# Kernel tuning notes

Measured on AMD Instinct MI355X. Metric: run time of the kernel, lower is better.

## Reference

```python
import jax, jax.numpy as jnp
import numpy as np

D_MODEL = 1024
N_HEADS = 16
D_K = D_MODEL // N_HEADS
BATCH = 8
SEQ = 1024
ROPE_BASE = 10000.0


def setup_inputs() -> dict:
    key = jax.random.key(0)
    ks = jax.random.split(key, 9)
    s = 1.0 / np.sqrt(D_MODEL)
    return {
        "x": jax.random.normal(ks[0], (BATCH, SEQ, D_MODEL), dtype=jnp.float32),
        "position_ids": jnp.arange(SEQ, dtype=jnp.int32)[None, :],
        "Wq": jax.random.normal(ks[1], (D_MODEL, D_MODEL), dtype=jnp.float32) * s,
        "bq": jnp.zeros((D_MODEL,), dtype=jnp.float32),
        "Wk": jax.random.normal(ks[2], (D_MODEL, D_MODEL), dtype=jnp.float32) * s,
        "bk": jnp.zeros((D_MODEL,), dtype=jnp.float32),
        "Wv": jax.random.normal(ks[3], (D_MODEL, D_MODEL), dtype=jnp.float32) * s,
        "bv": jnp.zeros((D_MODEL,), dtype=jnp.float32),
        "Wo": jax.random.normal(ks[4], (D_MODEL, D_MODEL), dtype=jnp.float32) * s,
        "bo": jnp.zeros((D_MODEL,), dtype=jnp.float32),
    }


def _apply_rope(t, position_ids):
    # t: [B, H, S, D_K]; position_ids: [1, S] (broadcast over batch)
    half = D_K // 2
    inv_freq = 1.0 / (ROPE_BASE ** (jnp.arange(half, dtype=jnp.float32) * 2.0 / D_K))
    ang = position_ids.astype(jnp.float32)[..., None] * inv_freq  # [1, S, half]
    cos = jnp.cos(ang)[:, None, :, :]  # [1, 1, S, half]
    sin = jnp.sin(ang)[:, None, :, :]
    t1, t2 = jnp.split(t, 2, axis=-1)
    return jnp.concatenate([t1 * cos - t2 * sin, t1 * sin + t2 * cos], axis=-1)


def reference(x, position_ids, Wq, bq, Wk, bk, Wv, bv, Wo, bo):
    B, S, D = x.shape
    def proj(W, b):
        # torch Linear: x @ W.T + b
        y = jnp.einsum('bsd,ed->bse', x, W) + b
        return y.reshape(B, S, N_HEADS, D_K).transpose(0, 2, 1, 3)  # [B,H,S,Dk]
    Q = proj(Wq, bq)
    K = proj(Wk, bk)
    V = proj(Wv, bv)
    Q = _apply_rope(Q, position_ids)
    K = _apply_rope(K, position_ids)
    scores = jnp.einsum('bhqd,bhkd->bhqk', Q, K) / jnp.sqrt(jnp.float32(D_K))
    attn = jax.nn.softmax(scores, axis=-1)
    out = jnp.einsum('bhqk,bhkd->bhqd', attn, V)
    out = out.transpose(0, 2, 1, 3).reshape(B, S, D)
    return jnp.einsum('bsd,ed->bse', out, Wo) + bo
```

## Files before the change

### kernel.cpp

```cpp
#include <hip/hip_runtime.h>
#include <hip/hip_bf16.h>


typedef __bf16 bf16_t;
typedef __bf16 bf16x8 __attribute__((ext_vector_type(8)));
typedef float  f32x4  __attribute__((ext_vector_type(4)));

static __device__ __forceinline__ f32x4 mfma16(bf16x8 a, bf16x8 b, f32x4 c) {
  return __builtin_amdgcn_mfma_f32_16x16x32_bf16(a, b, c, 0, 0, 0);
}

#if __has_builtin(__builtin_amdgcn_exp2f)
#define EXP2F(x) __builtin_amdgcn_exp2f(x)
#else
#define EXP2F(x) exp2f(x)
#endif

__global__ void k_prep(const float* __restrict__ x, const float* __restrict__ Wq,
                       const float* __restrict__ Wk, const float* __restrict__ Wv,
                       const float* __restrict__ Wo, const int* __restrict__ pos,
                       bf16_t* __restrict__ Xf, bf16_t* __restrict__ Wf,
                       float2* __restrict__ rt) {
  const int bid = blockIdx.x;
  const int t = threadIdx.x;
  if (bid < 4096) {
    int g = bid * 256 + t;
    int rg = g >> 11, kt = (g >> 6) & 31, lane = g & 63;
    int m = rg * 16 + (lane & 15);
    int k = kt * 32 + (lane >> 4) * 8;
    const float* s = x + (size_t)m * 1024 + k;
    float4 v0 = *(const float4*)s;
    float4 v1 = *(const float4*)(s + 4);
    union { bf16_t b[8]; } pk;
    pk.b[0] = (bf16_t)v0.x; pk.b[1] = (bf16_t)v0.y; pk.b[2] = (bf16_t)v0.z; pk.b[3] = (bf16_t)v0.w;
    pk.b[4] = (bf16_t)v1.x; pk.b[5] = (bf16_t)v1.y; pk.b[6] = (bf16_t)v1.z; pk.b[7] = (bf16_t)v1.w;
    __builtin_memcpy(Xf + (size_t)g * 8, pk.b, 16);
  } else if (bid < 6144) {
    int g = (bid - 4096) * 256 + t;
    int rg = g >> 11, kt = (g >> 6) & 31, lane = g & 63;
    const float* src = (rg < 64) ? Wq : (rg < 128) ? Wk : (rg < 192) ? Wv : Wo;
    int row = (rg & 63) * 16 + (lane & 15);
    int k = kt * 32 + (lane >> 4) * 8;
    const float* s = src + (size_t)row * 1024 + k;
    float4 v0 = *(const float4*)s;
    float4 v1 = *(const float4*)(s + 4);
    union { bf16_t b[8]; } pk;
    pk.b[0] = (bf16_t)v0.x; pk.b[1] = (bf16_t)v0.y; pk.b[2] = (bf16_t)v0.z; pk.b[3] = (bf16_t)v0.w;
    pk.b[4] = (bf16_t)v1.x; pk.b[5] = (bf16_t)v1.y; pk.b[6] = (bf16_t)v1.z; pk.b[7] = (bf16_t)v1.w;
    __builtin_memcpy(Wf + (size_t)g * 8, pk.b, 16);
  } else {
    int rb = bid - 6144;
    int s = rb * 8 + (t >> 5);
    int f = t & 31;
    float p = (float)pos[s];
    float inv = powf(10000.0f, -(float)(2 * f) / 64.0f);
    float a = p * inv;
    rt[s * 32 + f] = make_float2(cosf(a), sinf(a));
  }
}

#define GEMM_DIRECT_BODY(AfBase, BfBase)                                       \
  const int t = threadIdx.x;                                                   \
  const int lane = t & 63, w = t >> 6;                                         \
  const int hi = lane >> 4, c = lane & 15;                                     \
  const int wm = w >> 2, wn = w & 3;                                           \
  const bf16_t* Ab = (AfBase) + (size_t)((i0 >> 4) + wm * 4) * 16384 + lane * 8; \
  const bf16_t* Bb = (BfBase) + (size_t)((e0 >> 4) + wn * 4) * 16384 + lane * 8; \
  bf16x8 pa0, pa1, pa2, pa3, pb0, pb1, pb2, pb3;                               \
  bf16x8 qa0, qa1, qa2, qa3, qb0, qb1, qb2, qb3;                               \
  f32x4 acc[4][4] = {};                                                        \
  auto loadP = [&](int kt) {                                                   \
    pa0 = *(const bf16x8*)(Ab + kt * 512);                                     \
    pa1 = *(const bf16x8*)(Ab + 16384 + kt * 512);                             \
    pa2 = *(const bf16x8*)(Ab + 32768 + kt * 512);                             \
    pa3 = *(const bf16x8*)(Ab + 49152 + kt * 512);                             \
    pb0 = *(const bf16x8*)(Bb + kt * 512);                                     \
    pb1 = *(const bf16x8*)(Bb + 16384 + kt * 512);                             \
    pb2 = *(const bf16x8*)(Bb + 32768 + kt * 512);                             \
    pb3 = *(const bf16x8*)(Bb + 49152 + kt * 512);                             \
  };                                                                           \
  auto loadQ = [&](int kt) {                                                   \
    qa0 = *(const bf16x8*)(Ab + kt * 512);                                     \
    qa1 = *(const bf16x8*)(Ab + 16384 + kt * 512);                             \
    qa2 = *(const bf16x8*)(Ab + 32768 + kt * 512);                             \
    qa3 = *(const bf16x8*)(Ab + 49152 + kt * 512);                             \
    qb0 = *(const bf16x8*)(Bb + kt * 512);                                     \
    qb1 = *(const bf16x8*)(Bb + 16384 + kt * 512);                             \
    qb2 = *(const bf16x8*)(Bb + 32768 + kt * 512);                             \
    qb3 = *(const bf16x8*)(Bb + 49152 + kt * 512);                             \
  };                                                                           \
  auto compP = [&]() {                                                         \
    bf16x8 a_[4] = {pa0, pa1, pa2, pa3}, b_[4] = {pb0, pb1, pb2, pb3};         \
    __builtin_amdgcn_s_setprio(1);                                             \
    _Pragma("unroll") for (int fr = 0; fr < 4; ++fr)                           \
      _Pragma("unroll") for (int nc = 0; nc < 4; ++nc)                         \
        acc[fr][nc] = mfma16(a_[fr], b_[nc], acc[fr][nc]);                     \
    __builtin_amdgcn_s_setprio(0);                                             \
  };                                                                           \
  auto compQ = [&]() {                                                         \
    bf16x8 a_[4] = {qa0, qa1, qa2, qa3}, b_[4] = {qb0, qb1, qb2, qb3};         \
    __builtin_amdgcn_s_setprio(1);                                             \
    _Pragma("unroll") for (int fr = 0; fr < 4; ++fr)                           \
      _Pragma("unroll") for (int nc = 0; nc < 4; ++nc)                         \
        acc[fr][nc] = mfma16(a_[fr], b_[nc], acc[fr][nc]);                     \
    __builtin_amdgcn_s_setprio(0);                                             \
  };                                                                           \
  loadP(0);                                                                    \
  loadQ(1);                                                                    \
  _Pragma("unroll 3")                                                          \
  for (int jj = 0; jj < 15; ++jj) {                                            \
    compP(); loadP(jj * 2 + 2);                                                \
    compQ(); loadQ(jj * 2 + 3);                                                \
  }                                                                            \
  compP();                                                                     \
  compQ();

__global__ __launch_bounds__(512) void k_gemm_qkv(
    const bf16_t* __restrict__ Xf, const bf16_t* __restrict__ Wf,
    const float* __restrict__ bq, const float* __restrict__ bk,
    const float* __restrict__ bv, const float2* __restrict__ rt,
    bf16_t* __restrict__ Qh, bf16_t* __restrict__ Kg, bf16_t* __restrict__ Vg) {
  const int bid = blockIdx.x;
  const int x = bid & 7, q = bid >> 3;
  const int i0 = (x * 8 + (q & 7)) * 128;
  const int e0 = (q >> 3) * 256;

  GEMM_DIRECT_BODY(Xf, Wf)

  const int z = e0 >> 10;
  const int ez0 = (e0 & 1023) + wn * 64;
  const int h = ez0 >> 6;
  const float* bias = (z == 0) ? bq : (z == 1) ? bk : bv;
  if (z == 2) {
#pragma unroll
    for (int fr = 0; fr < 4; ++fr) {
      int i = i0 + wm * 64 + fr * 16 + hi * 4;
      int b_ = i >> 10, sbase = i & 1023;
      int bhv = b_ * 16 + h;
      int lane_ = c | (((sbase >> 3) & 3) << 4);
#pragma unroll
      for (int nc = 0; nc < 4; ++nc) {
        float bv_ = bias[ez0 + nc * 16 + c];
        union { bf16_t b[4]; } pk;
#pragma unroll
        for (int r = 0; r < 4; ++r) pk.b[r] = (bf16_t)(acc[fr][nc][r] + bv_);
        size_t g = (size_t)(bhv * 4 + nc) * 32 + (sbase >> 5);
        __builtin_memcpy(&Vg[g * 512 + lane_ * 8 + (sbase & 7)], pk.b, 8);
      }
    }
  } else if (z == 0) {
    const float scl = 0.18033688011112042f;
#pragma unroll
    for (int fr = 0; fr < 4; ++fr) {
      int i = i0 + wm * 64 + fr * 16 + hi * 4;
      int b_ = i >> 10, sbase = i & 1023;
      size_t obase = (size_t)((b_ * 16 + h) * 1024);
#pragma unroll
      for (int nc = 0; nc < 2; ++nc) {
        int f = nc * 16 + c;
        float b1_ = bias[ez0 + f], b2_ = bias[ez0 + f + 32];
#pragma unroll
        for (int r = 0; r < 4; ++r) {
          int s = sbase + r;
          float2 cs = rt[s * 32 + f];
          float q1 = acc[fr][nc][r] + b1_;
          float q2 = acc[fr][nc + 2][r] + b2_;
          Qh[(obase + s) * 64 + f] = (bf16_t)((q1 * cs.x - q2 * cs.y) * scl);
          Qh[(obase + s) * 64 + f + 32] = (bf16_t)((q1 * cs.y + q2 * cs.x) * scl);
        }
      }
    }
  } else {
#pragma unroll
    for (int fr = 0; fr < 4; ++fr) {
      int i = i0 + wm * 64 + fr * 16 + hi * 4;
      int b_ = i >> 10, sbase = i & 1023;
      bf16_t* gb = Kg + (size_t)((b_ * 16 + h) * 64 + (sbase >> 4)) * 1024;
#pragma unroll
      for (int nc = 0; nc < 2; ++nc) {
        int f = nc * 16 + c;
        float b1_ = bias[ez0 + f], b2_ = bias[ez0 + f + 32];
        int laneHi = (nc * 2 + (c >> 3)) << 4;
#pragma unroll
        for (int r = 0; r < 4; ++r) {
          int s = sbase + r;
          float2 cs = rt[s * 32 + f];
          float q1 = acc[fr][nc][r] + b1_;
          float q2 = acc[fr][nc + 2][r] + b2_;
          size_t off = (size_t)((hi * 4 + r) | laneHi) * 8 + (c & 7);
          gb[off] = (bf16_t)(q1 * cs.x - q2 * cs.y);
          gb[off + 512] = (bf16_t)(q1 * cs.y + q2 * cs.x);
        }
      }
    }
  }
}

__global__ __launch_bounds__(512) void k_gemm_out(
    const bf16_t* __restrict__ Ogf, const bf16_t* __restrict__ Wf,
    const float* __restrict__ bo, float* __restrict__ out) {
  const int bid = blockIdx.x;
  const int x = bid & 7, q = bid >> 3;
  const int i0 = (x * 8 + (q & 7)) * 128;
  const int e0 = (q >> 3) * 256;
  const bf16_t* WfO = Wf + (size_t)192 * 16384;

  GEMM_DIRECT_BODY(Ogf, WfO)

#pragma unroll
  for (int fr = 0; fr < 4; ++fr) {
    int i = i0 + wm * 64 + fr * 16 + hi * 4;
#pragma unroll
    for (int nc = 0; nc < 4; ++nc) {
      int e = e0 + wn * 64 + nc * 16 + c;
      float bv_ = bo[e];
#pragma unroll
      for (int r = 0; r < 4; ++r)
        out[(size_t)(i + r) * 1024 + e] = acc[fr][nc][r] + bv_;
    }
  }
}

__global__ __launch_bounds__(512) void k_attn(
    const bf16_t* __restrict__ Qh, const bf16_t* __restrict__ Kg,
    const bf16_t* __restrict__ Vg, bf16_t* __restrict__ Ogf) {
  __shared__ alignas(16) char PL[8][2048];
  const int t = threadIdx.x;
  const int lane = t & 63, w = t >> 6;
  const int hi = lane >> 4, c = lane & 15;
  const int bid = blockIdx.x;
  const int wg = (bid & 7) * 32 + (bid >> 3);
  const int bh = wg >> 1, half = wg & 1;
  const int q0 = half * 512 + w * 64;
  const size_t qbase = (size_t)bh * 64 * 1024;

  const bf16_t* Kb = Kg + (size_t)bh * 65536 + lane * 8;
  const bf16_t* Vb = Vg + (size_t)bh * 65536 + lane * 8;

  bf16x8 qf[4][2];
#pragma unroll
  for (int ss = 0; ss < 4; ++ss)
#pragma unroll
    for (int kk = 0; kk < 2; ++kk)
      qf[ss][kk] = *(const bf16x8*)&Qh[qbase + (size_t)(q0 + ss * 16 + c) * 64 +
                                       kk * 32 + hi * 8];

  f32x4 o[4][4] = {};
  float m_[4] = {-1e30f, -1e30f, -1e30f, -1e30f};
  float l_[4] = {0.f, 0.f, 0.f, 0.f};
  char* const plw = &PL[w][0];

  bf16x8 kp[8], kq[8], vv[8];
#pragma unroll
  for (int i = 0; i < 8; ++i) kp[i] = *(const bf16x8*)(Kb + i * 512);

#define SM_PV(ST, M, L, O)                                                     \
  {                                                                            \
    float pmax = -1e30f;                                                       \
    _Pragma("unroll") for (int ni = 0; ni < 4; ++ni)                           \
      _Pragma("unroll") for (int r = 0; r < 4; ++r)                            \
        pmax = fmaxf(pmax, ST[ni][r]);                                         \
    pmax = fmaxf(pmax, __shfl_xor(pmax, 16));                                  \
    pmax = fmaxf(pmax, __shfl_xor(pmax, 32));                                  \
    if (!__all(pmax <= M + 8.0f)) {                 \
      float mn = fmaxf(M, pmax);                                               \
      float sc = EXP2F(M - mn);                                                \
      M = mn;                                                                  \
      L *= sc;                                                                 \
      _Pragma("unroll") for (int od = 0; od < 4; ++od)                         \
        _Pragma("unroll") for (int r = 0; r < 4; ++r) O[od][r] *= sc;          \
    }                                                                          \
    float psum = 0.f;                                                          \
    _Pragma("unroll") for (int ni = 0; ni < 4; ++ni) {                         \
      union { bf16_t b[4]; } pk;                                               \
      _Pragma("unroll") for (int r = 0; r < 4; ++r) {                          \
        float p = EXP2F(ST[ni][r] - M);                                        \
        psum += p;                                                             \
        pk.b[r] = (bf16_t)p;                                                   \
      }                                                                        \
      __builtin_memcpy(plw + (ni * 2 + (hi >> 1)) * 256 + c * 16 + (hi & 1) * 8, \
                       pk.b, 8);                                               \
    }                                                                          \
    psum += __shfl_xor(psum, 16);                                              \
    psum += __shfl_xor(psum, 32);                                              \
    L += psum;                                                                 \
    bf16x8 pa[2];                                                              \
    __builtin_memcpy(&pa[0], plw + lane * 16, 16);                             \
    __builtin_memcpy(&pa[1], plw + 1024 + lane * 16, 16);                      \
    _Pragma("unroll") for (int od = 0; od < 4; ++od)                           \
      _Pragma("unroll") for (int kk = 0; kk < 2; ++kk)                         \
        O[od] = mfma16(vv[od * 2 + kk], pa[kk], O[od]);                        \
  }

#define ATTN_TILE(KS, KN, KT)                                                  \
  {                                                                            \
    _Pragma("unroll") for (int i = 0; i < 8; ++i)                              \
      vv[i] = *(const bf16x8*)(Vb + ((i >> 1) * 32 + (KT) * 2 + (i & 1)) * 512); \
    _Pragma("unroll") for (int ss = 0; ss < 4; ++ss) {                         \
      f32x4 st[4] = {};                                                        \
      _Pragma("unroll") for (int ni = 0; ni < 4; ++ni)                         \
        _Pragma("unroll") for (int kk = 0; kk < 2; ++kk)                       \
          st[ni] = mfma16(KS[ni * 2 + kk], qf[ss][kk], st[ni]);                \
      if (ss == 0 && (KT) + 1 < 16) {                                          \
        _Pragma("unroll") for (int i = 0; i < 8; ++i)                          \
          KN[i] = *(const bf16x8*)(Kb + (((KT) + 1) * 8 + i) * 512);           \
      }                                                                        \
      SM_PV(st, m_[ss], l_[ss], o[ss])                                         \
    }                                                                          \
  }

  for (int jj = 0; jj < 8; ++jj) {
    ATTN_TILE(kp, kq, jj * 2);
    ATTN_TILE(kq, kp, jj * 2 + 1);
  }
#undef ATTN_TILE
#undef SM_PV

  int b_ = bh >> 4, h = bh & 15;
  int rg0 = ((b_ << 10) + q0) >> 4;
#pragma unroll
  for (int ss = 0; ss < 4; ++ss) {
    float iv = 1.f / l_[ss];
#pragma unroll
    for (int od = 0; od < 4; ++od) {
      union { bf16_t b[4]; } pk;
#pragma unroll
      for (int r = 0; r < 4; ++r) pk.b[r] = (bf16_t)(o[ss][od][r] * iv);
      int kt2 = (h << 1) + (od >> 1);
      int lp = ((od & 1) * 2 + (hi >> 1)) * 16 + c;
      int el = (hi & 1) * 4;
      __builtin_memcpy(&Ogf[((size_t)((rg0 + ss) * 32 + kt2) * 64 + lp) * 8 + el],
                       pk.b, 8);
    }
  }
}

extern "C" void kernel_launch(void* const* d_in, const int* in_sizes, int n_in,
                              void* d_out, int out_size, void* d_ws, size_t ws_size,
                              hipStream_t stream) {
  const float* x = (const float*)d_in[0];
  const int* pos = (const int*)d_in[1];
  const float* Wq = (const float*)d_in[2];
  const float* bq = (const float*)d_in[3];
  const float* Wk = (const float*)d_in[4];
  const float* bk = (const float*)d_in[5];
  const float* Wv = (const float*)d_in[6];
  const float* bv = (const float*)d_in[7];
  const float* Wo = (const float*)d_in[8];
  const float* bo = (const float*)d_in[9];
  float* out = (float*)d_out;

  char* ws = (char*)d_ws;
  bf16_t* Xf = (bf16_t*)ws;
  bf16_t* Wf = (bf16_t*)(ws + (16u << 20));
  bf16_t* Vg = (bf16_t*)(ws + (24u << 20));
  float2* rt = (float2*)(ws + (42u << 20));
  bf16_t* Qh = (bf16_t*)d_out;
  bf16_t* Kg = (bf16_t*)d_out + (size_t)8 * 1024 * 1024;
  bf16_t* Ogf = Xf;

  k_prep<<<6272, 256, 0, stream>>>(x, Wq, Wk, Wv, Wo, pos, Xf, Wf, rt);
  k_gemm_qkv<<<768, 512, 0, stream>>>(Xf, Wf, bq, bk, bv, rt, Qh, Kg, Vg);
  k_attn<<<256, 512, 0, stream>>>(Qh, Kg, Vg, Ogf);
  k_gemm_out<<<256, 512, 0, stream>>>(Ogf, Wf, bo, out);
}
```

Measured before the change: 143.5 us.

## Widen per-warp GEMM tile to 128x64 with 4-warp 256x128 blocks

Reshapes the direct-load MFMA GEMMs so each warp computes 8x4 fragments (128x64) instead of 4x4, with 4 warps per block covering a 256x128 tile. Each B fragment loaded from global memory is now reused across twice as many A fragments, which cuts global load traffic per MFMA. In exchange, register pressure roughly doubles for accumulators and prefetch buffers, and there are half as many threads per block, which may reduce occupancy and latency hiding.

```diff
diff --git a/kernel.cpp b/kernel.cpp
--- a/kernel.cpp
+++ b/kernel.cpp
@@ -59,50 +59,39 @@
   }
 }
 
-#define GEMM_DIRECT_BODY(AfBase, BfBase)                                       \
+#define GEMM_WIDE_BODY(AfBase, BfBase)                                         \
   const int t = threadIdx.x;                                                   \
-  const int lane = t & 63, w = t >> 6;                                         \
+  const int lane = t & 63, w = t >> 6;                         \
   const int hi = lane >> 4, c = lane & 15;                                     \
-  const int wm = w >> 2, wn = w & 3;                                           \
-  const bf16_t* Ab = (AfBase) + (size_t)((i0 >> 4) + wm * 4) * 16384 + lane * 8; \
+  const int wm = w >> 1, wn = w & 1;                                           \
+  const bf16_t* Ab = (AfBase) + (size_t)((i0 >> 4) + wm * 8) * 16384 + lane * 8; \
   const bf16_t* Bb = (BfBase) + (size_t)((e0 >> 4) + wn * 4) * 16384 + lane * 8; \
-  bf16x8 pa0, pa1, pa2, pa3, pb0, pb1, pb2, pb3;                               \
-  bf16x8 qa0, qa1, qa2, qa3, qb0, qb1, qb2, qb3;                               \
-  f32x4 acc[4][4] = {};                                                        \
+  bf16x8 pA[8], pB[4], qA[8], qB[4];                                           \
+  f32x4 acc[8][4] = {};                                                        \
   auto loadP = [&](int kt) {                                                   \
-    pa0 = *(const bf16x8*)(Ab + kt * 512);                                     \
-    pa1 = *(const bf16x8*)(Ab + 16384 + kt * 512);                             \
-    pa2 = *(const bf16x8*)(Ab + 32768 + kt * 512);                             \
-    pa3 = *(const bf16x8*)(Ab + 49152 + kt * 512);                             \
-    pb0 = *(const bf16x8*)(Bb + kt * 512);                                     \
-    pb1 = *(const bf16x8*)(Bb + 16384 + kt * 512);                             \
-    pb2 = *(const bf16x8*)(Bb + 32768 + kt * 512);                             \
-    pb3 = *(const bf16x8*)(Bb + 49152 + kt * 512);                             \
+    _Pragma("unroll") for (int f = 0; f < 8; ++f)                              \
+      pA[f] = *(const bf16x8*)(Ab + (size_t)f * 16384 + kt * 512);             \
+    _Pragma("unroll") for (int f = 0; f < 4; ++f)                              \
+      pB[f] = *(const bf16x8*)(Bb + (size_t)f * 16384 + kt * 512);             \
   };                                                                           \
   auto loadQ = [&](int kt) {                                                   \
-    qa0 = *(const bf16x8*)(Ab + kt * 512);                                     \
-    qa1 = *(const bf16x8*)(Ab + 16384 + kt * 512);                             \
-    qa2 = *(const bf16x8*)(Ab + 32768 + kt * 512);                             \
-    qa3 = *(const bf16x8*)(Ab + 49152 + kt * 512);                             \
-    qb0 = *(const bf16x8*)(Bb + kt * 512);                                     \
-    qb1 = *(const bf16x8*)(Bb + 16384 + kt * 512);                             \
-    qb2 = *(const bf16x8*)(Bb + 32768 + kt * 512);                             \
-    qb3 = *(const bf16x8*)(Bb + 49152 + kt * 512);                             \
+    _Pragma("unroll") for (int f = 0; f < 8; ++f)                              \
+      qA[f] = *(const bf16x8*)(Ab + (size_t)f * 16384 + kt * 512);             \
+    _Pragma("unroll") for (int f = 0; f < 4; ++f)                              \
+      qB[f] = *(const bf16x8*)(Bb + (size_t)f * 16384 + kt * 512);             \
   };                                                                           \
   auto compP = [&]() {                                                         \
-    bf16x8 a_[4] = {pa0, pa1, pa2, pa3}, b_[4] = {pb0, pb1, pb2, pb3};         \
     __builtin_amdgcn_s_setprio(1);                                             \
-    _Pragma("unroll") for (int fr = 0; fr < 4; ++fr)                           \
+    _Pragma("unroll") for (int fr = 0; fr < 8; ++fr)                           \
       _Pragma("unroll") for (int nc = 0; nc < 4; ++nc)                         \
-        acc[fr][nc] = mfma16(a_[fr], b_[nc], acc[fr][nc]);                     \
+        acc[fr][nc] = mfma16(pA[fr], pB[nc], acc[fr][nc]);                     \
     __builtin_amdgcn_s_setprio(0);                                             \
   };                                                                           \
   auto compQ = [&]() {                                                         \
-    bf16x8 a_[4] = {qa0, qa1, qa2, qa3}, b_[4] = {qb0, qb1, qb2, qb3};         \
     __builtin_amdgcn_s_setprio(1);                                             \
-    _Pragma("unroll") for (int fr = 0; fr < 4; ++fr)                           \
+    _Pragma("unroll") for (int fr = 0; fr < 8; ++fr)                           \
       _Pragma("unroll") for (int nc = 0; nc < 4; ++nc)                         \
-        acc[fr][nc] = mfma16(a_[fr], b_[nc], acc[fr][nc]);                     \
+        acc[fr][nc] = mfma16(qA[fr], qB[nc], acc[fr][nc]);                     \
     __builtin_amdgcn_s_setprio(0);                                             \
   };                                                                           \
   loadP(0);                                                                    \
@@ -115,17 +104,17 @@
   compP();                                                                     \
   compQ();
 
-__global__ __launch_bounds__(512) void k_gemm_qkv(
+__global__ __launch_bounds__(256) void k_gemm_qkv(
     const bf16_t* __restrict__ Xf, const bf16_t* __restrict__ Wf,
     const float* __restrict__ bq, const float* __restrict__ bk,
     const float* __restrict__ bv, const float2* __restrict__ rt,
     bf16_t* __restrict__ Qh, bf16_t* __restrict__ Kg, bf16_t* __restrict__ Vg) {
   const int bid = blockIdx.x;
   const int x = bid & 7, q = bid >> 3;
-  const int i0 = (x * 8 + (q & 7)) * 128;
-  const int e0 = (q >> 3) * 256;
-
-  GEMM_DIRECT_BODY(Xf, Wf)
+  const int i0 = (x * 4 + (q & 3)) * 256;
+  const int e0 = (q >> 2) * 128;
+
+  GEMM_WIDE_BODY(Xf, Wf)
 
   const int z = e0 >> 10;
   const int ez0 = (e0 & 1023) + wn * 64;
@@ -133,8 +122,8 @@
   const float* bias = (z == 0) ? bq : (z == 1) ? bk : bv;
   if (z == 2) {
 #pragma unroll
-    for (int fr = 0; fr < 4; ++fr) {
-      int i = i0 + wm * 64 + fr * 16 + hi * 4;
+    for (int fr = 0; fr < 8; ++fr) {
+      int i = i0 + wm * 128 + fr * 16 + hi * 4;
       int b_ = i >> 10, sbase = i & 1023;
       int bhv = b_ * 16 + h;
       int lane_ = c | (((sbase >> 3) & 3) << 4);
@@ -151,8 +140,8 @@
   } else if (z == 0) {
     const float scl = 0.18033688011112042f;
 #pragma unroll
-    for (int fr = 0; fr < 4; ++fr) {
-      int i = i0 + wm * 64 + fr * 16 + hi * 4;
+    for (int fr = 0; fr < 8; ++fr) {
+      int i = i0 + wm * 128 + fr * 16 + hi * 4;
       int b_ = i >> 10, sbase = i & 1023;
       size_t obase = (size_t)((b_ * 16 + h) * 1024);
 #pragma unroll
@@ -172,8 +161,8 @@
     }
   } else {
 #pragma unroll
-    for (int fr = 0; fr < 4; ++fr) {
-      int i = i0 + wm * 64 + fr * 16 + hi * 4;
+    for (int fr = 0; fr < 8; ++fr) {
+      int i = i0 + wm * 128 + fr * 16 + hi * 4;
       int b_ = i >> 10, sbase = i & 1023;
       bf16_t* gb = Kg + (size_t)((b_ * 16 + h) * 64 + (sbase >> 4)) * 1024;
 #pragma unroll
@@ -196,20 +185,20 @@
   }
 }
 
-__global__ __launch_bounds__(512) void k_gemm_out(
+__global__ __launch_bounds__(256) void k_gemm_out(
     const bf16_t* __restrict__ Ogf, const bf16_t* __restrict__ Wf,
     const float* __restrict__ bo, float* __restrict__ out) {
   const int bid = blockIdx.x;
   const int x = bid & 7, q = bid >> 3;
-  const int i0 = (x * 8 + (q & 7)) * 128;
-  const int e0 = (q >> 3) * 256;
+  const int i0 = (x * 4 + (q & 3)) * 256;
+  const int e0 = (q >> 2) * 128;
   const bf16_t* WfO = Wf + (size_t)192 * 16384;
 
-  GEMM_DIRECT_BODY(Ogf, WfO)
-
-#pragma unroll
-  for (int fr = 0; fr < 4; ++fr) {
-    int i = i0 + wm * 64 + fr * 16 + hi * 4;
+  GEMM_WIDE_BODY(Ogf, WfO)
+
+#pragma unroll
+  for (int fr = 0; fr < 8; ++fr) {
+    int i = i0 + wm * 128 + fr * 16 + hi * 4;
 #pragma unroll
     for (int nc = 0; nc < 4; ++nc) {
       int e = e0 + wn * 64 + nc * 16 + c;
@@ -360,7 +349,7 @@
   bf16_t* Ogf = Xf;
 
   k_prep<<<6272, 256, 0, stream>>>(x, Wq, Wk, Wv, Wo, pos, Xf, Wf, rt);
-  k_gemm_qkv<<<768, 512, 0, stream>>>(Xf, Wf, bq, bk, bv, rt, Qh, Kg, Vg);
+  k_gemm_qkv<<<768, 256, 0, stream>>>(Xf, Wf, bq, bk, bv, rt, Qh, Kg, Vg);
   k_attn<<<256, 512, 0, stream>>>(Qh, Kg, Vg, Ogf);
-  k_gemm_out<<<256, 512, 0, stream>>>(Ogf, Wf, bo, out);
-}
+  k_gemm_out<<<256, 256, 0, stream>>>(Ogf, Wf, bo, out);
+}
```

After: 133.7 us. 6.8% less time.
